# Optimization experiments

Measured on AMD Instinct MI355X. Metric: run time of the kernel, lower is better.

The kernel has to match this reference:

```python
import jax, jax.numpy as jnp
import numpy as np

B, J, D, H, EH, L, W = 64, 16384, 32, 128, 256, 32, 4
LN_EPS = 1e-5
TEMP = 1.0


def _ln(x, g, b):
    mu = x.mean(-1, keepdims=True)
    var = x.var(-1, keepdims=True)
    return (x - mu) / jnp.sqrt(var + LN_EPS) * g + b


def setup_inputs() -> dict:
    key = jax.random.key(0)
    ks = jax.random.split(key, 24)
    n = jax.random.normal
    inp = {
        'x': n(ks[0], (B, J), jnp.float32),
        'mask': jax.random.randint(ks[1], (B, J), 0, 2).astype(jnp.int32),
        'feat_emb': n(ks[2], (J, D), jnp.float32),
        'h_w1': n(ks[3], (1 + D, H), jnp.float32) / np.sqrt(1 + D),
        'h_b1': jnp.zeros((H,), jnp.float32),
        'h_ln1_g': jnp.ones((H,), jnp.float32),
        'h_ln1_b': jnp.zeros((H,), jnp.float32),
        'h_w2': n(ks[4], (H, D), jnp.float32) / np.sqrt(H),
        'h_b2': jnp.zeros((D,), jnp.float32),
        'h_ln2_g': jnp.ones((D,), jnp.float32),
        'h_ln2_b': jnp.zeros((D,), jnp.float32),
        'g_w1': n(ks[5], (D, D // 2), jnp.float32) / np.sqrt(D),
        'g_b1': jnp.zeros((D // 2,), jnp.float32),
        'g_w2': n(ks[6], (D // 2, W), jnp.float32) / np.sqrt(D // 2),
        'g_b2': jnp.zeros((W,), jnp.float32),
        'c_w': n(ks[7], (W * D, D), jnp.float32) / np.sqrt(W * D),
        'c_b': jnp.zeros((D,), jnp.float32),
        'c_ln_g': jnp.ones((D,), jnp.float32),
        'c_ln_b': jnp.zeros((D,), jnp.float32),
        'e_w1': n(ks[8], (D, EH), jnp.float32) / np.sqrt(D),
        'e_b1': jnp.zeros((EH,), jnp.float32),
        'e_ln1_g': jnp.ones((EH,), jnp.float32),
        'e_ln1_b': jnp.zeros((EH,), jnp.float32),
        'e_w2': n(ks[9], (EH, 2 * L), jnp.float32) / np.sqrt(EH),
        'e_b2': jnp.zeros((2 * L,), jnp.float32),
        'e_ln2_g': jnp.ones((2 * L,), jnp.float32),
        'e_ln2_b': jnp.zeros((2 * L,), jnp.float32),
    }
    return inp


def reference(x, mask, feat_emb, h_w1, h_b1, h_ln1_g, h_ln1_b, h_w2, h_b2,
              h_ln2_g, h_ln2_b, g_w1, g_b1, g_w2, g_b2, c_w, c_b, c_ln_g,
              c_ln_b, e_w1, e_b1, e_ln1_g, e_ln1_b, e_w2, e_b2, e_ln2_g,
              e_ln2_b):
    m = mask.astype(bool)  # (B,J)
    # h_layer on all (b,j) pairs; unobserved rows are excluded via masked softmax
    h_in = jnp.concatenate([x[..., None], jnp.broadcast_to(feat_emb, (x.shape[0], J, D))], axis=-1)  # (B,J,1+D)
    h = jax.nn.relu(_ln(h_in @ h_w1 + h_b1, h_ln1_g, h_ln1_b))  # (B,J,H)
    h_out = jax.nn.relu(_ln(h @ h_w2 + h_b2, h_ln2_g, h_ln2_b))  # (B,J,D)
    raw = jax.nn.relu(h_out @ g_w1 + g_b1) @ g_w2 + g_b2  # (B,J,W)
    logits = jnp.clip(raw * TEMP, -10.0, 10.0)
    # masked softmax over observed junctions, per head
    logits_m = jnp.where(m[..., None], logits, -1e9)
    ex = jnp.exp(logits_m - logits_m.max(axis=1, keepdims=True)) * m[..., None]
    wts = ex / jnp.maximum(ex.sum(axis=1, keepdims=True), 1e-30)  # (B,J,W)
    head_sums = jnp.einsum('bjw,bjd->bwd', wts, h_out).reshape(x.shape[0], W * D)
    combined = jax.nn.relu(_ln(head_sums @ c_w + c_b, c_ln_g, c_ln_b))  # (B,D)
    has_obs = m.any(axis=1)
    c = jnp.where(has_obs[:, None], combined, 0.0)
    e1 = jax.nn.relu(_ln(c @ e_w1 + e_b1, e_ln1_g, e_ln1_b))
    mu_logvar = jax.nn.relu(_ln(e1 @ e_w2 + e_b2, e_ln2_g, e_ln2_b))  # (B,2L)
    mu, logvar = jnp.split(mu_logvar, 2, axis=-1)
    return mu, logvar
```

## Files before the change

kernel.cpp:

```cpp
#include <hip/hip_runtime.h>
#include <hip/hip_bf16.h>
#include <math.h>

#define BB 64
#define JJ 16384
#define DD 32
#define HH 128
#define WW 4
#define EHH 256
#define CHUNK 64
#define CPB 16
#define NBLK 16
#define NPART (NBLK * 4)
#define PART_STRIDE 136
#define LN_EPS 1e-5f
#define HPRE_OFF  (4 << 20)
#define HSTAT_OFF (HPRE_OFF + JJ*HH*4)
#define SQ_OFF    (HSTAT_OFF + JJ*16)

#define COMP(q,e) ((e)==0?(q).x:((e)==1?(q).y:((e)==2?(q).z:(q).w)))

#define FMAQ(acc,B,q,f) \
  acc[B+0]=fmaf((q).x,f,acc[B+0]); acc[B+1]=fmaf((q).y,f,acc[B+1]); \
  acc[B+2]=fmaf((q).z,f,acc[B+2]); acc[B+3]=fmaf((q).w,f,acc[B+3]);

__global__ void pe_k0(const float* __restrict__ feat, const float* __restrict__ w1,
                      const float* __restrict__ b1,
                      float* __restrict__ hpre, float4* __restrict__ hstat4)
{
    const int tid = threadIdx.x;
    const int row = blockIdx.x * 32 + (tid >> 3);
    const int sg = tid & 7;
    float acc[16];
    #pragma unroll
    for (int o = 0; o < 16; ++o) acc[o] = 0.f;
    const float* fr = feat + (size_t)row * 32;
    const float* w1s = w1 + sg * 16;
    #pragma unroll 4
    for (int k = 0; k < 32; ++k) {
        const float f = fr[k];
        const float* wr = w1s + (k + 1) * HH;
        const float4 q0 = *(const float4*)(wr);
        const float4 q1 = *(const float4*)(wr + 4);
        const float4 q2 = *(const float4*)(wr + 8);
        const float4 q3 = *(const float4*)(wr + 12);
        FMAQ(acc,0,q0,f) FMAQ(acc,4,q1,f) FMAQ(acc,8,q2,f) FMAQ(acc,12,q3,f)
    }
    #pragma unroll
    for (int i = 0; i < 4; ++i) {
        const float4 bq = *(const float4*)(b1 + sg*16 + 4*i);
        acc[4*i+0]+=bq.x; acc[4*i+1]+=bq.y; acc[4*i+2]+=bq.z; acc[4*i+3]+=bq.w;
    }
    float s0p=0.f, q0p=0.f, q1p=0.f;
    #pragma unroll
    for (int o = 0; o < 16; ++o) {
        s0p += acc[o];
        q0p = fmaf(acc[o], acc[o], q0p);
        q1p = fmaf(acc[o], w1s[o], q1p);
    }
    #pragma unroll
    for (int st = 1; st < 8; st <<= 1) {
        s0p += __shfl_xor(s0p, st, 64);
        q0p += __shfl_xor(q0p, st, 64);
        q1p += __shfl_xor(q1p, st, 64);
    }
    if (sg == 0) hstat4[row] = make_float4(s0p, q0p, q1p, 0.f);

    float4* op = (float4*)(hpre + (size_t)row * HH + sg * 16);
    op[0] = make_float4(acc[0],acc[1],acc[2],acc[3]);
    op[1] = make_float4(acc[4],acc[5],acc[6],acc[7]);
    op[2] = make_float4(acc[8],acc[9],acc[10],acc[11]);
    op[3] = make_float4(acc[12],acc[13],acc[14],acc[15]);
}

__global__ void pe_k0s(const float* __restrict__ w1, float* __restrict__ sq)
{
    const int t = threadIdx.x;
    float w = w1[t];
    float s = w, q = w * w;
    #pragma unroll
    for (int st = 1; st < 64; st <<= 1) {
        s += __shfl_xor(s, st, 64);
        q += __shfl_xor(q, st, 64);
    }
    __shared__ float ls[4];
    if ((t & 63) == 0) { ls[(t>>6)*2] = s; ls[(t>>6)*2+1] = q; }
    __syncthreads();
    if (t == 0) { sq[0] = ls[0] + ls[2]; sq[1] = ls[1] + ls[3]; }
}

__launch_bounds__(256, 2)
__global__ void pe_k1(const float* __restrict__ x, const int* __restrict__ mask,
                      const float* __restrict__ hpre,
                      const float4* __restrict__ hstat4, const float* __restrict__ sq,
                      const float* __restrict__ w1,
                      const float* __restrict__ ln1g, const float* __restrict__ ln1b,
                      const float* __restrict__ w2, const float* __restrict__ b2,
                      const float* __restrict__ ln2g, const float* __restrict__ ln2b,
                      const float* __restrict__ gw1, const float* __restrict__ gb1,
                      const float* __restrict__ gw2, const float* __restrict__ gb2,
                      float* __restrict__ part)
{
    const int tid = threadIdx.x;
    const int cb = blockIdx.x, b = blockIdx.y;
    const int rg = tid >> 3, sg = tid & 7;
    const int r0 = rg * 2, r1 = r0 + 1;
    const int wv = tid >> 6, lane = tid & 63;

    __shared__ float4 uni[CHUNK * 17];
    __shared__ float4 p_lds4[CHUNK];
    __shared__ float4 w2l[HH * 8];

    const int ad = lane & 31, half = lane >> 5;
    const int wa = half, wb = half + 2;
    const int rbase = wv * 16;

    float m_run_a = -1e30f, s_run_a = 0.f, accr_a = 0.f;
    float m_run_b = -1e30f, s_run_b = 0.f, accr_b = 0.f;

    const float* w1s = w1 + sg * 16;
    const float S1v = sq[0], Q2v = sq[1];

    {
        const float4* w2g = (const float4*)w2;
        #pragma unroll
        for (int i = 0; i < 4; ++i) w2l[tid + i*256] = w2g[tid + i*256];
    }
    __syncthreads();

    for (int ch = 0; ch < CPB; ++ch) {
        const int jbase = (cb * CPB + ch) * CHUNK;

        float hb0[16], hb1[16];
        const float2 xq = *(const float2*)(x + (size_t)b * JJ + jbase + r0);
        {
            const float4* hp4 = (const float4*)(hpre + (size_t)jbase * HH);
            #pragma unroll
            for (int i = 0; i < 4; ++i) {
                const float4 h0q = hp4[r0*32 + sg*4 + i];
                const float4 h1q = hp4[r1*32 + sg*4 + i];
                const float4 wq = *(const float4*)(w1s + 4*i);
                hb0[4*i+0] = fmaf(wq.x, xq.x, h0q.x);
                hb0[4*i+1] = fmaf(wq.y, xq.x, h0q.y);
                hb0[4*i+2] = fmaf(wq.z, xq.x, h0q.z);
                hb0[4*i+3] = fmaf(wq.w, xq.x, h0q.w);
                hb1[4*i+0] = fmaf(wq.x, xq.y, h1q.x);
                hb1[4*i+1] = fmaf(wq.y, xq.y, h1q.y);
                hb1[4*i+2] = fmaf(wq.z, xq.y, h1q.z);
                hb1[4*i+3] = fmaf(wq.w, xq.y, h1q.w);
            }
        }
        {
            const float4 st0 = hstat4[jbase + r0];
            const float4 st1 = hstat4[jbase + r1];
            const float mu0 = (st0.x + xq.x * S1v) * (1.f/HH);
            const float e20 = (st0.y + 2.f*xq.x*st0.z + xq.x*xq.x*Q2v) * (1.f/HH);
            const float rs0 = rsqrtf(fmaxf(e20 - mu0*mu0, 0.f) + LN_EPS);
            const float mu1 = (st1.x + xq.y * S1v) * (1.f/HH);
            const float e21 = (st1.y + 2.f*xq.y*st1.z + xq.y*xq.y*Q2v) * (1.f/HH);
            const float rs1 = rsqrtf(fmaxf(e21 - mu1*mu1, 0.f) + LN_EPS);
            #pragma unroll
            for (int q4 = 0; q4 < 4; ++q4) {
                const float4 gq = *(const float4*)(ln1g + sg*16 + q4*4);
                const float4 tq = *(const float4*)(ln1b + sg*16 + q4*4);
                hb0[q4*4+0]=fmaxf(fmaf((hb0[q4*4+0]-mu0)*rs0, gq.x, tq.x),0.f);
                hb0[q4*4+1]=fmaxf(fmaf((hb0[q4*4+1]-mu0)*rs0, gq.y, tq.y),0.f);
                hb0[q4*4+2]=fmaxf(fmaf((hb0[q4*4+2]-mu0)*rs0, gq.z, tq.z),0.f);
                hb0[q4*4+3]=fmaxf(fmaf((hb0[q4*4+3]-mu0)*rs0, gq.w, tq.w),0.f);
                hb1[q4*4+0]=fmaxf(fmaf((hb1[q4*4+0]-mu1)*rs1, gq.x, tq.x),0.f);
                hb1[q4*4+1]=fmaxf(fmaf((hb1[q4*4+1]-mu1)*rs1, gq.y, tq.y),0.f);
                hb1[q4*4+2]=fmaxf(fmaf((hb1[q4*4+2]-mu1)*rs1, gq.z, tq.z),0.f);
                hb1[q4*4+3]=fmaxf(fmaf((hb1[q4*4+3]-mu1)*rs1, gq.w, tq.w),0.f);
            }
        }

        float ac0[4] = {0.f,0.f,0.f,0.f}, ac1[4] = {0.f,0.f,0.f,0.f};
        #pragma unroll
        for (int hf2 = 0; hf2 < 2; ++hf2) {
            if ((sg >> 2) == hf2) {
                const int sgl = sg & 3;
                #pragma unroll
                for (int o4 = 0; o4 < 4; ++o4) {
                    const int p = (sgl*4 + o4 + rg) & 15;
                    uni[r0*17 + p] = make_float4(hb0[o4*4],hb0[o4*4+1],hb0[o4*4+2],hb0[o4*4+3]);
                    uni[r1*17 + p] = make_float4(hb1[o4*4],hb1[o4*4+1],hb1[o4*4+2],hb1[o4*4+3]);
                }
            }
            #pragma unroll 4
            for (int L = 0; L < 16; ++L) {
                const int p = (L + rg) & 15;
                const float4 h0q = uni[r0*17 + p];
                const float4 h1q = uni[r1*17 + p];
                #pragma unroll
                for (int e = 0; e < 4; ++e) {
                    const float4 wq = w2l[(hf2*64 + L*4 + e)*8 + sg];
                    const float h0 = COMP(h0q,e), h1 = COMP(h1q,e);
                    ac0[0]=fmaf(h0,wq.x,ac0[0]); ac1[0]=fmaf(h1,wq.x,ac1[0]);
                    ac0[1]=fmaf(h0,wq.y,ac0[1]); ac1[1]=fmaf(h1,wq.y,ac1[1]);
                    ac0[2]=fmaf(h0,wq.z,ac0[2]); ac1[2]=fmaf(h1,wq.z,ac1[2]);
                    ac0[3]=fmaf(h0,wq.w,ac0[3]); ac1[3]=fmaf(h1,wq.w,ac1[3]);
                }
            }
        }
        {
            const float4 bq = *(const float4*)(b2 + sg*4);
            ac0[0]+=bq.x; ac0[1]+=bq.y; ac0[2]+=bq.z; ac0[3]+=bq.w;
            ac1[0]+=bq.x; ac1[1]+=bq.y; ac1[2]+=bq.z; ac1[3]+=bq.w;
        }
        {
            float s0 = ac0[0]+ac0[1]+ac0[2]+ac0[3];
            float s1 = ac1[0]+ac1[1]+ac1[2]+ac1[3];
            float q0 = ac0[0]*ac0[0]+ac0[1]*ac0[1]+ac0[2]*ac0[2]+ac0[3]*ac0[3];
            float q1 = ac1[0]*ac1[0]+ac1[1]*ac1[1]+ac1[2]*ac1[2]+ac1[3]*ac1[3];
            #pragma unroll
            for (int st = 1; st < 8; st <<= 1) {
                s0 += __shfl_xor(s0, st, 64); q0 += __shfl_xor(q0, st, 64);
                s1 += __shfl_xor(s1, st, 64); q1 += __shfl_xor(q1, st, 64);
            }
            const float mu0 = s0 * (1.f/DD);
            const float rs0 = rsqrtf(fmaxf(q0*(1.f/DD) - mu0*mu0, 0.f) + LN_EPS);
            const float mu1 = s1 * (1.f/DD);
            const float rs1 = rsqrtf(fmaxf(q1*(1.f/DD) - mu1*mu1, 0.f) + LN_EPS);
            const float4 gq = *(const float4*)(ln2g + sg*4);
            const float4 tq = *(const float4*)(ln2b + sg*4);
            uni[r0*17 + sg] = make_float4(
                fmaxf(fmaf((ac0[0]-mu0)*rs0, gq.x, tq.x),0.f),
                fmaxf(fmaf((ac0[1]-mu0)*rs0, gq.y, tq.y),0.f),
                fmaxf(fmaf((ac0[2]-mu0)*rs0, gq.z, tq.z),0.f),
                fmaxf(fmaf((ac0[3]-mu0)*rs0, gq.w, tq.w),0.f));
            uni[r1*17 + sg] = make_float4(
                fmaxf(fmaf((ac1[0]-mu1)*rs1, gq.x, tq.x),0.f),
                fmaxf(fmaf((ac1[1]-mu1)*rs1, gq.y, tq.y),0.f),
                fmaxf(fmaf((ac1[2]-mu1)*rs1, gq.z, tq.z),0.f),
                fmaxf(fmaf((ac1[3]-mu1)*rs1, gq.w, tq.w),0.f));
        }

        float g1r0[2] = {0.f, 0.f}, g1r1[2] = {0.f, 0.f};
        #pragma unroll
        for (int k4 = 0; k4 < 8; ++k4) {
            const float4 h0q = uni[r0*17 + k4];
            const float4 h1q = uni[r1*17 + k4];
            #pragma unroll
            for (int e = 0; e < 4; ++e) {
                const float2 wq = *(const float2*)(gw1 + (k4*4+e)*16 + sg*2);
                const float h0 = COMP(h0q,e), h1 = COMP(h1q,e);
                g1r0[0]=fmaf(h0,wq.x,g1r0[0]); g1r0[1]=fmaf(h0,wq.y,g1r0[1]);
                g1r1[0]=fmaf(h1,wq.x,g1r1[0]); g1r1[1]=fmaf(h1,wq.y,g1r1[1]);
            }
        }
        {
            const float2 gbq = *(const float2*)(gb1 + sg*2);
            g1r0[0]=fmaxf(g1r0[0]+gbq.x,0.f); g1r0[1]=fmaxf(g1r0[1]+gbq.y,0.f);
            g1r1[0]=fmaxf(g1r1[0]+gbq.x,0.f); g1r1[1]=fmaxf(g1r1[1]+gbq.y,0.f);
        }

        float l0[4], l1[4];
        {
            const float4 w0q = *(const float4*)(gw2 + (sg*2)*4);
            const float4 w1q = *(const float4*)(gw2 + (sg*2+1)*4);
            l0[0]=fmaf(g1r0[0],w0q.x, g1r0[1]*w1q.x);
            l0[1]=fmaf(g1r0[0],w0q.y, g1r0[1]*w1q.y);
            l0[2]=fmaf(g1r0[0],w0q.z, g1r0[1]*w1q.z);
            l0[3]=fmaf(g1r0[0],w0q.w, g1r0[1]*w1q.w);
            l1[0]=fmaf(g1r1[0],w0q.x, g1r1[1]*w1q.x);
            l1[1]=fmaf(g1r1[0],w0q.y, g1r1[1]*w1q.y);
            l1[2]=fmaf(g1r1[0],w0q.z, g1r1[1]*w1q.z);
            l1[3]=fmaf(g1r1[0],w0q.w, g1r1[1]*w1q.w);
            #pragma unroll
            for (int st = 1; st < 8; st <<= 1) {
                #pragma unroll
                for (int w = 0; w < 4; ++w) {
                    l0[w] += __shfl_xor(l0[w], st, 64);
                    l1[w] += __shfl_xor(l1[w], st, 64);
                }
            }
            const float4 gbq = *(const float4*)gb2;
            l0[0] = fminf(fmaxf(l0[0]+gbq.x, -10.f), 10.f);
            l0[1] = fminf(fmaxf(l0[1]+gbq.y, -10.f), 10.f);
            l0[2] = fminf(fmaxf(l0[2]+gbq.z, -10.f), 10.f);
            l0[3] = fminf(fmaxf(l0[3]+gbq.w, -10.f), 10.f);
            l1[0] = fminf(fmaxf(l1[0]+gbq.x, -10.f), 10.f);
            l1[1] = fminf(fmaxf(l1[1]+gbq.y, -10.f), 10.f);
            l1[2] = fminf(fmaxf(l1[2]+gbq.z, -10.f), 10.f);
            l1[3] = fminf(fmaxf(l1[3]+gbq.w, -10.f), 10.f);
        }

        const int2 mq = *(const int2*)(mask + (size_t)b * JJ + jbase + r0);
        const float mk0 = mq.x ? 1.f : 0.f, mk1 = mq.y ? 1.f : 0.f;
        float lm[4];
        #pragma unroll
        for (int w = 0; w < 4; ++w)
            lm[w] = fmaxf(mk0 > 0.f ? l0[w] : -1e30f,
                          mk1 > 0.f ? l1[w] : -1e30f);
        #pragma unroll
        for (int st = 8; st < 64; st <<= 1) {
            #pragma unroll
            for (int w = 0; w < 4; ++w)
                lm[w] = fmaxf(lm[w], __shfl_xor(lm[w], st, 64));
        }

        float ps[4];
        {
            float p0v[4], p1v[4];
            #pragma unroll
            for (int w = 0; w < 4; ++w) {
                p0v[w] = mk0 * __expf(fminf(l0[w] - lm[w], 0.f));
                p1v[w] = mk1 * __expf(fminf(l1[w] - lm[w], 0.f));
                ps[w] = p0v[w] + p1v[w];
            }
            if (sg == 0) {
                p_lds4[r0] = make_float4(p0v[0],p0v[1],p0v[2],p0v[3]);
                p_lds4[r1] = make_float4(p1v[0],p1v[1],p1v[2],p1v[3]);
            }
            #pragma unroll
            for (int st = 8; st < 64; st <<= 1) {
                #pragma unroll
                for (int w = 0; w < 4; ++w) ps[w] += __shfl_xor(ps[w], st, 64);
            }
        }

        {
            float dota = 0.f, dotb = 0.f;
            #pragma unroll 8
            for (int rr = 0; rr < 16; ++rr) {
                const float hval = ((const float*)&uni[(rbase+rr)*17])[ad];
                const float* pr = (const float*)&p_lds4[rbase+rr];
                dota = fmaf(pr[wa], hval, dota);
                dotb = fmaf(pr[wb], hval, dotb);
            }
            const float mna = fmaxf(m_run_a, lm[wa]);
            const float eaa = __expf(m_run_a - mna);
            const float eba = __expf(lm[wa] - mna);
            accr_a  = fmaf(accr_a,  eaa, dota * eba);
            s_run_a = fmaf(s_run_a, eaa, ps[wa] * eba);
            m_run_a = mna;
            const float mnb = fmaxf(m_run_b, lm[wb]);
            const float eab = __expf(m_run_b - mnb);
            const float ebb = __expf(lm[wb] - mnb);
            accr_b  = fmaf(accr_b,  eab, dotb * ebb);
            s_run_b = fmaf(s_run_b, eab, ps[wb] * ebb);
            m_run_b = mnb;
        }
    }

    {
        float* pp = part + (size_t)((b * NBLK + cb) * 4 + wv) * PART_STRIDE;
        if (ad == 0) {
            pp[wa] = m_run_a; pp[4 + wa] = s_run_a;
            pp[wb] = m_run_b; pp[4 + wb] = s_run_b;
        }
        pp[8 + wa*32 + ad] = accr_a;
        pp[8 + wb*32 + ad] = accr_b;
    }
}

__global__ void pe_k2(const float* __restrict__ part,
                      const float* __restrict__ cw, const float* __restrict__ cb_,
                      const float* __restrict__ cg, const float* __restrict__ cbn,
                      const float* __restrict__ ew1, const float* __restrict__ eb1,
                      const float* __restrict__ eg1, const float* __restrict__ ebn1,
                      const float* __restrict__ ew2, const float* __restrict__ eb2,
                      const float* __restrict__ eg2, const float* __restrict__ ebn2,
                      float* __restrict__ out)
{
    const int b = blockIdx.x, tid = threadIdx.x;
    const int w = tid >> 5, d = tid & 31;
    __shared__ float hs[128];
    __shared__ float cbuf[32];
    __shared__ float ebuf[256];
    __shared__ float obuf[64];

    float m = -1e30f, s = 0.f, a = 0.f;
    for (int c = 0; c < NPART; ++c) {
        const float* pp = part + (size_t)(b * NPART + c) * PART_STRIDE;
        const float mc = pp[w], sc = pp[4 + w], ac = pp[8 + w*32 + d];
        const float mn = fmaxf(m, mc);
        const float e0 = __expf(m - mn), e1v = __expf(mc - mn);
        a = fmaf(a, e0, ac * e1v);
        s = fmaf(s, e0, sc * e1v);
        m = mn;
    }
    hs[w*32 + d] = a / fmaxf(s, 1e-30f);
    const bool has = (s > 0.f);
    __syncthreads();

    if (tid < 32) {
        float acc = cb_[tid];
        for (int k = 0; k < 128; ++k) acc = fmaf(hs[k], cw[k*32 + tid], acc);
        cbuf[tid] = acc;
    }
    __syncthreads();
    {
        float mu = 0.f, sq = 0.f;
        for (int k = 0; k < 32; ++k) { float v = cbuf[k]; mu += v; sq = fmaf(v, v, sq); }
        mu *= (1.f/32);
        float var = fmaxf(sq*(1.f/32) - mu*mu, 0.f);
        const float rs = rsqrtf(var + LN_EPS);
        __syncthreads();
        if (tid < 32) {
            float v = (cbuf[tid] - mu) * rs;
            v = fmaxf(fmaf(v, cg[tid], cbn[tid]), 0.f);
            cbuf[tid] = has ? v : 0.f;
        }
    }
    __syncthreads();

    #pragma unroll
    for (int r = 0; r < 2; ++r) {
        const int o = tid + r*128;
        float acc = eb1[o];
        for (int k = 0; k < 32; ++k) acc = fmaf(cbuf[k], ew1[k*EHH + o], acc);
        ebuf[o] = acc;
    }
    __syncthreads();
    {
        float mu = 0.f, sq = 0.f;
        for (int k = 0; k < 256; ++k) { float v = ebuf[k]; mu += v; sq = fmaf(v, v, sq); }
        mu *= (1.f/256);
        float var = fmaxf(sq*(1.f/256) - mu*mu, 0.f);
        const float rs = rsqrtf(var + LN_EPS);
        __syncthreads();
        #pragma unroll
        for (int r = 0; r < 2; ++r) {
            const int o = tid + r*128;
            float v = (ebuf[o] - mu) * rs;
            ebuf[o] = fmaxf(fmaf(v, eg1[o], ebn1[o]), 0.f);
        }
    }
    __syncthreads();

    if (tid < 64) {
        float acc = eb2[tid];
        for (int k = 0; k < 256; ++k) acc = fmaf(ebuf[k], ew2[k*64 + tid], acc);
        obuf[tid] = acc;
    }
    __syncthreads();
    {
        float mu = 0.f, sq = 0.f;
        for (int k = 0; k < 64; ++k) { float v = obuf[k]; mu += v; sq = fmaf(v, v, sq); }
        mu *= (1.f/64);
        float var = fmaxf(sq*(1.f/64) - mu*mu, 0.f);
        const float rs = rsqrtf(var + LN_EPS);
        if (tid < 64) {
            float v = (obuf[tid] - mu) * rs;
            v = fmaxf(fmaf(v, eg2[tid], ebn2[tid]), 0.f);
            if (tid < 32) out[(size_t)b*32 + tid] = v;
            else          out[(size_t)BB*32 + (size_t)b*32 + (tid-32)] = v;
        }
    }
}

extern "C" void kernel_launch(void* const* d_in, const int* in_sizes, int n_in,
                              void* d_out, int out_size, void* d_ws, size_t ws_size,
                              hipStream_t stream) {
    (void)in_sizes; (void)n_in; (void)out_size; (void)ws_size;
    const float* x     = (const float*)d_in[0];
    const int*   mask  = (const int*)  d_in[1];
    const float* feat  = (const float*)d_in[2];
    const float* h_w1  = (const float*)d_in[3];
    const float* h_b1  = (const float*)d_in[4];
    const float* h_l1g = (const float*)d_in[5];
    const float* h_l1b = (const float*)d_in[6];
    const float* h_w2  = (const float*)d_in[7];
    const float* h_b2  = (const float*)d_in[8];
    const float* h_l2g = (const float*)d_in[9];
    const float* h_l2b = (const float*)d_in[10];
    const float* g_w1  = (const float*)d_in[11];
    const float* g_b1  = (const float*)d_in[12];
    const float* g_w2  = (const float*)d_in[13];
    const float* g_b2  = (const float*)d_in[14];
    const float* c_w   = (const float*)d_in[15];
    const float* c_b   = (const float*)d_in[16];
    const float* c_lg  = (const float*)d_in[17];
    const float* c_lb  = (const float*)d_in[18];
    const float* e_w1  = (const float*)d_in[19];
    const float* e_b1  = (const float*)d_in[20];
    const float* e_l1g = (const float*)d_in[21];
    const float* e_l1b = (const float*)d_in[22];
    const float* e_w2  = (const float*)d_in[23];
    const float* e_b2  = (const float*)d_in[24];
    const float* e_l2g = (const float*)d_in[25];
    const float* e_l2b = (const float*)d_in[26];

    float*  part   = (float*)d_ws;
    float*  hpre   = (float*)((char*)d_ws + HPRE_OFF);
    float4* hstat4 = (float4*)((char*)d_ws + HSTAT_OFF);
    float*  sqv    = (float*)((char*)d_ws + SQ_OFF);
    float*  out    = (float*)d_out;

    pe_k0<<<dim3(JJ / 32), dim3(256), 0, stream>>>(feat, h_w1, h_b1, hpre, hstat4);
    pe_k0s<<<dim3(1), dim3(128), 0, stream>>>(h_w1, sqv);

    dim3 g1(NBLK, BB);
    pe_k1<<<g1, dim3(256), 0, stream>>>(x, mask, hpre, hstat4, sqv,
                                        h_w1, h_l1g, h_l1b,
                                        h_w2, h_b2, h_l2g, h_l2b,
                                        g_w1, g_b1, g_w2, g_b2, part);
    pe_k2<<<dim3(BB), dim3(128), 0, stream>>>(part,
                                              c_w, c_b, c_lg, c_lb,
                                              e_w1, e_b1, e_l1g, e_l1b,
                                              e_w2, e_b2, e_l2g, e_l2b, out);
}
```

Baseline: 331.2 us.

## Split w2 reads between LDS and global, use nontemporal hpre loads

In the second h-layer matmul, half of the w2 weight rows are now read straight from global memory (through the cache) while the other half still come from LDS. The aim is to spread operand traffic between the LDS and vector-memory paths. The precomputed hpre loads become nontemporal so this large streamed array does not evict reused data from cache. The COMP component-select macro is replaced with explicit unrolled FMAs in both small matmuls. This adds global-load latency inside the inner loop.

```diff
diff --git a/kernel.cpp b/kernel.cpp
--- a/kernel.cpp
+++ b/kernel.cpp
@@ -18,11 +18,17 @@
 #define HSTAT_OFF (HPRE_OFF + JJ*HH*4)
 #define SQ_OFF    (HSTAT_OFF + JJ*16)
 
-#define COMP(q,e) ((e)==0?(q).x:((e)==1?(q).y:((e)==2?(q).z:(q).w)))
+typedef float vf4 __attribute__((ext_vector_type(4)));
 
 #define FMAQ(acc,B,q,f) \
   acc[B+0]=fmaf((q).x,f,acc[B+0]); acc[B+1]=fmaf((q).y,f,acc[B+1]); \
   acc[B+2]=fmaf((q).z,f,acc[B+2]); acc[B+3]=fmaf((q).w,f,acc[B+3]);
+
+#define S2FMA(wq,h0,h1) \
+  ac0[0]=fmaf(h0,(wq).x,ac0[0]); ac1[0]=fmaf(h1,(wq).x,ac1[0]); \
+  ac0[1]=fmaf(h0,(wq).y,ac0[1]); ac1[1]=fmaf(h1,(wq).y,ac1[1]); \
+  ac0[2]=fmaf(h0,(wq).z,ac0[2]); ac1[2]=fmaf(h1,(wq).z,ac1[2]); \
+  ac0[3]=fmaf(h0,(wq).w,ac0[3]); ac1[3]=fmaf(h1,(wq).w,ac1[3]);
 
 __global__ void pe_k0(const float* __restrict__ feat, const float* __restrict__ w1,
                       const float* __restrict__ b1,
@@ -134,11 +140,11 @@
         float hb0[16], hb1[16];
         const float2 xq = *(const float2*)(x + (size_t)b * JJ + jbase + r0);
         {
-            const float4* hp4 = (const float4*)(hpre + (size_t)jbase * HH);
+            const vf4* hp4 = (const vf4*)(hpre + (size_t)jbase * HH);
             #pragma unroll
             for (int i = 0; i < 4; ++i) {
-                const float4 h0q = hp4[r0*32 + sg*4 + i];
-                const float4 h1q = hp4[r1*32 + sg*4 + i];
+                const vf4 h0q = __builtin_nontemporal_load(&hp4[r0*32 + sg*4 + i]);
+                const vf4 h1q = __builtin_nontemporal_load(&hp4[r1*32 + sg*4 + i]);
                 const float4 wq = *(const float4*)(w1s + 4*i);
                 hb0[4*i+0] = fmaf(wq.x, xq.x, h0q.x);
                 hb0[4*i+1] = fmaf(wq.y, xq.x, h0q.y);
@@ -191,14 +197,23 @@
                 const int p = (L + rg) & 15;
                 const float4 h0q = uni[r0*17 + p];
                 const float4 h1q = uni[r1*17 + p];
-                #pragma unroll
-                for (int e = 0; e < 4; ++e) {
-                    const float4 wq = w2l[(hf2*64 + L*4 + e)*8 + sg];
-                    const float h0 = COMP(h0q,e), h1 = COMP(h1q,e);
-                    ac0[0]=fmaf(h0,wq.x,ac0[0]); ac1[0]=fmaf(h1,wq.x,ac1[0]);
-                    ac0[1]=fmaf(h0,wq.y,ac0[1]); ac1[1]=fmaf(h1,wq.y,ac1[1]);
-                    ac0[2]=fmaf(h0,wq.z,ac0[2]); ac1[2]=fmaf(h1,wq.z,ac1[2]);
-                    ac0[3]=fmaf(h0,wq.w,ac0[3]); ac1[3]=fmaf(h1,wq.w,ac1[3]);
+                const int kb = hf2*64 + L*4;
+                const float* w2g = w2 + (size_t)kb*DD + sg*4;
+                {
+                    const float4 wq = w2l[(kb + 0)*8 + sg];
+                    S2FMA(wq, h0q.x, h1q.x)
+                }
+                {
+                    const float4 wq = w2l[(kb + 1)*8 + sg];
+                    S2FMA(wq, h0q.y, h1q.y)
+                }
+                {
+                    const float4 wq = *(const float4*)(w2g + 2*DD);
+                    S2FMA(wq, h0q.z, h1q.z)
+                }
+                {
+                    const float4 wq = *(const float4*)(w2g + 3*DD);
+                    S2FMA(wq, h0q.w, h1q.w)
                 }
             }
         }
@@ -240,13 +255,20 @@
         for (int k4 = 0; k4 < 8; ++k4) {
             const float4 h0q = uni[r0*17 + k4];
             const float4 h1q = uni[r1*17 + k4];
-            #pragma unroll
-            for (int e = 0; e < 4; ++e) {
-                const float2 wq = *(const float2*)(gw1 + (k4*4+e)*16 + sg*2);
-                const float h0 = COMP(h0q,e), h1 = COMP(h1q,e);
-                g1r0[0]=fmaf(h0,wq.x,g1r0[0]); g1r0[1]=fmaf(h0,wq.y,g1r0[1]);
-                g1r1[0]=fmaf(h1,wq.x,g1r1[0]); g1r1[1]=fmaf(h1,wq.y,g1r1[1]);
-            }
+            const float h0a = h0q.x, h0b = h0q.y, h0c = h0q.z, h0d = h0q.w;
+            const float h1a = h1q.x, h1b = h1q.y, h1c = h1q.z, h1d = h1q.w;
+            const float2 w0 = *(const float2*)(gw1 + (k4*4+0)*16 + sg*2);
+            const float2 w1q = *(const float2*)(gw1 + (k4*4+1)*16 + sg*2);
+            const float2 w2q = *(const float2*)(gw1 + (k4*4+2)*16 + sg*2);
+            const float2 w3q = *(const float2*)(gw1 + (k4*4+3)*16 + sg*2);
+            g1r0[0]=fmaf(h0a,w0.x,g1r0[0]); g1r0[1]=fmaf(h0a,w0.y,g1r0[1]);
+            g1r1[0]=fmaf(h1a,w0.x,g1r1[0]); g1r1[1]=fmaf(h1a,w0.y,g1r1[1]);
+            g1r0[0]=fmaf(h0b,w1q.x,g1r0[0]); g1r0[1]=fmaf(h0b,w1q.y,g1r0[1]);
+            g1r1[0]=fmaf(h1b,w1q.x,g1r1[0]); g1r1[1]=fmaf(h1b,w1q.y,g1r1[1]);
+            g1r0[0]=fmaf(h0c,w2q.x,g1r0[0]); g1r0[1]=fmaf(h0c,w2q.y,g1r0[1]);
+            g1r1[0]=fmaf(h1c,w2q.x,g1r1[0]); g1r1[1]=fmaf(h1c,w2q.y,g1r1[1]);
+            g1r0[0]=fmaf(h0d,w3q.x,g1r0[0]); g1r0[1]=fmaf(h0d,w3q.y,g1r0[1]);
+            g1r1[0]=fmaf(h1d,w3q.x,g1r1[0]); g1r1[1]=fmaf(h1d,w3q.y,g1r1[1]);
         }
         {
             const float2 gbq = *(const float2*)(gb1 + sg*2);
```

Result: slower. 421.9 us (+27.4%).
